# Performance work log

Hardware: AMD Instinct MI355X
Metric: run time of the kernel (lower is better)

The kernel has to match this reference:

```python
import jax, jax.numpy as jnp
import numpy as np

B, S, I, H = 64, 2048, 256, 256


def setup_inputs() -> dict:
    key = jax.random.key(0)
    ks = jax.random.split(key, 13)
    s_i = 1.0 / np.sqrt(I)
    s_h = 1.0 / np.sqrt(H)
    inp = {
        "input_seq": jax.random.normal(ks[0], (B, S, I), dtype=jnp.float32),
        "Wz": jax.random.uniform(ks[1], (I, H), jnp.float32, -s_i, s_i),
        "bz": jax.random.uniform(ks[2], (H,), jnp.float32, -s_i, s_i),
        "Wr": jax.random.uniform(ks[3], (I, H), jnp.float32, -s_i, s_i),
        "br": jax.random.uniform(ks[4], (H,), jnp.float32, -s_i, s_i),
        "Wh": jax.random.uniform(ks[5], (I, H), jnp.float32, -s_i, s_i),
        "bh": jax.random.uniform(ks[6], (H,), jnp.float32, -s_i, s_i),
        "Uz": jax.random.uniform(ks[7], (H, H), jnp.float32, -s_h, s_h),
        "buz": jax.random.uniform(ks[8], (H,), jnp.float32, -s_h, s_h),
        "Ur": jax.random.uniform(ks[9], (H, H), jnp.float32, -s_h, s_h),
        "bur": jax.random.uniform(ks[10], (H,), jnp.float32, -s_h, s_h),
        "Uh": jax.random.uniform(ks[11], (H, H), jnp.float32, -s_h, s_h),
        "buh": jax.random.uniform(ks[12], (H,), jnp.float32, -s_h, s_h),
    }
    return inp


def reference(input_seq, Wz, bz, Wr, br, Wh, bh, Uz, buz, Ur, bur, Uh, buh):
    # Precompute all input-side GEMMs in one batched pass: [B,S,H] each
    xz = jnp.einsum("bsi,ih->bsh", input_seq, Wz) + bz
    xr = jnp.einsum("bsi,ih->bsh", input_seq, Wr) + br
    xh = jnp.einsum("bsi,ih->bsh", input_seq, Wh) + bh
    # Time-major for scan: [S,B,H]
    xs = (xz.transpose(1, 0, 2), xr.transpose(1, 0, 2), xh.transpose(1, 0, 2))

    def step(h_prev, x_t):
        xz_t, xr_t, xh_t = x_t
        z = jax.nn.sigmoid(xz_t + h_prev @ Uz + buz)
        r = jax.nn.sigmoid(xr_t + h_prev @ Ur + bur)
        cand = jnp.tanh(xh_t + r * (h_prev @ Uh + buh))
        h_t = (1.0 - z) * h_prev + z * cand
        return h_t, h_t

    h0 = jnp.zeros((input_seq.shape[0], Uz.shape[0]), dtype=input_seq.dtype)
    _, hs = jax.lax.scan(step, h0, xs)  # hs: [S,B,H]
    return hs.transpose(1, 0, 2)  # [B,S,H]
```

## Files before the change

### kernel.cpp

```cpp
#include <hip/hip_runtime.h>
#include <hip/hip_bf16.h>
#include <hip/hip_fp16.h>


#define S_LEN 2048
#define BATCH 64
#define HDIM  256
#define NGATE 768
#define M_TOTAL (BATCH * S_LEN)

typedef _Float16 h8_t __attribute__((ext_vector_type(8)));
typedef float    f32x4 __attribute__((ext_vector_type(4)));
typedef int      i32x4 __attribute__((ext_vector_type(4)));

static __device__ __forceinline__ float h2f(unsigned short s) {
    _Float16 h; __builtin_memcpy(&h, &s, 2); return (float)h;
}
static __device__ __forceinline__ unsigned short f2h(float f) {
    _Float16 h = (_Float16)f; unsigned short s; __builtin_memcpy(&s, &h, 2); return s;
}

static __device__ __forceinline__ float sigmoid_fast(float x) {
    float e = __builtin_amdgcn_exp2f(-1.44269504088896341f * x);
    return __builtin_amdgcn_rcpf(1.0f + e);
}
static __device__ __forceinline__ float tanh_fast(float x) {
    return 2.0f * sigmoid_fast(2.0f * x) - 1.0f;
}


__global__ void k_cvt_x(const float4* __restrict__ x4, ushort4* __restrict__ xh4) {
    int i = blockIdx.x * blockDim.x + threadIdx.x;
    float4 v = x4[i];
    ushort4 o;
    o.x = f2h(v.x); o.y = f2h(v.y); o.z = f2h(v.z); o.w = f2h(v.w);
    xh4[i] = o;
}

__global__ void k_prep_w(const float* __restrict__ Wz, const float* __restrict__ Wr,
                         const float* __restrict__ Wh,
                         const float* __restrict__ bz, const float* __restrict__ br,
                         const float* __restrict__ bh,
                         const float* __restrict__ buz, const float* __restrict__ bur,
                         unsigned short* __restrict__ Wt, float* __restrict__ biascat) {
    int n = blockIdx.x;
    int k = threadIdx.x;
    int g = n >> 8, h = n & 255;
    const float* W = (g == 0) ? Wz : (g == 1) ? Wr : Wh;
    Wt[n * 256 + k] = f2h(W[k * 256 + h]);
    if (k == 0) {
        float bias = (g == 0) ? (bz[h] + buz[h]) : (g == 1) ? (br[h] + bur[h]) : bh[h];
        biascat[n] = bias;
    }
}

__global__ void k_prep_uq(const float* __restrict__ Uz, const float* __restrict__ Ur,
                          const float* __restrict__ Uh,
                          signed char* __restrict__ Ufrag, float* __restrict__ invU) {
    int blk = blockIdx.x;
    int g = blk >> 8, col = blk & 255;
    int k = threadIdx.x;
    const float* U = (g == 0) ? Uz : (g == 1) ? Ur : Uh;
    float v = U[k * 256 + col];
    __shared__ float red[256];
    red[k] = fabsf(v);
    __syncthreads();
    for (int off = 128; off > 0; off >>= 1) {
        if (k < off) red[k] = fmaxf(red[k], red[k + off]);
        __syncthreads();
    }
    float m = red[0];
    float s = (m > 0.0f) ? 127.0f / m : 0.0f;
    int q = __float2int_rn(v * s);
    q = max(-127, min(127, q));
    int ks = k >> 6, l4 = (k >> 4) & 3, e = k & 15;
    int l = l4 * 16 + (col & 15), nt = col >> 4;
    Ufrag[((size_t)(((g * 16 + nt) * 4 + ks) * 64 + l)) * 16 + e] = (signed char)q;
    if (k == 0) invU[g * 256 + col] = m * (1.0f / 16129.0f);
}


#define LDT 264

__global__ __launch_bounds__(256) void k_gemm_x(const unsigned short* __restrict__ Xh,
                                                const unsigned short* __restrict__ Wt,
                                                const float* __restrict__ biascat,
                                                unsigned short* __restrict__ XG) {
    __shared__ unsigned short As[128 * LDT];
    __shared__ unsigned short Bs[128 * LDT];
    int tid = threadIdx.x;
    int m0 = blockIdx.x * 128;
    int n0 = blockIdx.y * 128;

    {
        const unsigned short* ga = Xh + (size_t)m0 * 256;
        const unsigned short* gb = Wt + (size_t)n0 * 256;
#pragma unroll
        for (int i = 0; i < 16; i++) {
            int chunk = tid + i * 256;
            int row = chunk >> 5;
            int c8  = (chunk & 31) * 8;
            uint4 va = *(const uint4*)(ga + row * 256 + c8);
            *(uint4*)(As + row * LDT + c8) = va;
            uint4 vb = *(const uint4*)(gb + row * 256 + c8);
            *(uint4*)(Bs + row * LDT + c8) = vb;
        }
    }
    __syncthreads();

    int lane = tid & 63, wv = tid >> 6;
    int mw = (wv & 1) * 64, nw = (wv >> 1) * 64;
    int lr = lane & 15, lg = lane >> 4;

    f32x4 acc[4][4] = {};
#pragma unroll
    for (int k = 0; k < 8; k++) {
        h8_t a[4], b[4];
#pragma unroll
        for (int i = 0; i < 4; i++)
            a[i] = *(const h8_t*)(As + (mw + i * 16 + lr) * LDT + k * 32 + lg * 8);
#pragma unroll
        for (int jj = 0; jj < 4; jj++)
            b[jj] = *(const h8_t*)(Bs + (nw + jj * 16 + lr) * LDT + k * 32 + lg * 8);
#pragma unroll
        for (int i = 0; i < 4; i++)
#pragma unroll
            for (int jj = 0; jj < 4; jj++)
                acc[i][jj] = __builtin_amdgcn_mfma_f32_16x16x32_f16(a[i], b[jj], acc[i][jj], 0, 0, 0);
    }

#pragma unroll
    for (int jj = 0; jj < 4; jj++) {
        int gcol = n0 + nw + jj * 16 + lr;
        float bias = biascat[gcol];
#pragma unroll
        for (int i = 0; i < 4; i++) {
            int grow = m0 + mw + i * 16 + lg * 4;
#pragma unroll
            for (int r = 0; r < 4; r++) {
                XG[(size_t)(grow + r) * NGATE + gcol] = f2h(acc[i][jj][r] + bias);
            }
        }
    }
}


__global__ __launch_bounds__(512) __attribute__((amdgpu_waves_per_eu(2, 2)))
void k_gru(const i32x4* __restrict__ Ufrag,
           const float* __restrict__ invU,
           const unsigned short* __restrict__ XG,
           const float* __restrict__ buh,
           float* __restrict__ out) {
    __shared__ __align__(16) signed char hb[2][256];
    int tid = threadIdx.x;
    int lane = tid & 63, w = tid >> 6;
    int l4 = lane >> 4, lc = lane & 15;
    int b = blockIdx.x;
    int sel = l4 & 1;
    int c = (2 * w + sel) * 16 + lc;
    bool writer = (l4 < 2);

    i32x4 uf[3][2][4];
#pragma unroll
    for (int g = 0; g < 3; g++)
#pragma unroll
        for (int i = 0; i < 2; i++)
#pragma unroll
            for (int ks = 0; ks < 4; ks++)
                uf[g][i][ks] = Ufrag[(size_t)((g * 16 + (2 * w + i)) * 4 + ks) * 64 + lane];
#pragma unroll
    for (int g = 0; g < 3; g++)
#pragma unroll
        for (int i = 0; i < 2; i++)
#pragma unroll
            for (int ks = 0; ks < 4; ks++)
                asm volatile("" : "+v"(uf[g][i][ks]));

    i32x4 zc = {};
    asm volatile("" : "+v"(zc));

    float invz = invU[0 * 256 + c], invr = invU[1 * 256 + c], invh = invU[2 * 256 + c];
    float buh_c = buh[c];

    if (tid < 64) ((int*)hb[0])[tid] = 0;

    const unsigned short* xb = XG + (size_t)b * S_LEN * NGATE;
    float* ob = out + (size_t)b * S_LEN * HDIM;

    const unsigned short* xp = xb + c;
    unsigned short pz = xp[0], pr = xp[256], ph = xp[512];
    xp += NGATE;
    float hm = 0.0f;
    __syncthreads();

    for (int t = 0; t < S_LEN; ++t) {
        const signed char* hrow = hb[t & 1];
        signed char* hdst = hb[(t & 1) ^ 1];

        i32x4 acc[3][2];
        __builtin_amdgcn_s_setprio(1);
        {
            i32x4 a = *(const i32x4*)(hrow + l4 * 16);
#pragma unroll
            for (int g = 0; g < 3; g++)
#pragma unroll
                for (int i = 0; i < 2; i++)
                    acc[g][i] = __builtin_amdgcn_mfma_i32_16x16x64_i8(a, uf[g][i][0], zc, 0, 0, 0);
        }
#pragma unroll
        for (int ks = 1; ks < 4; ks++) {
            i32x4 a = *(const i32x4*)(hrow + ks * 64 + l4 * 16);
#pragma unroll
            for (int g = 0; g < 3; g++)
#pragma unroll
                for (int i = 0; i < 2; i++)
                    acc[g][i] = __builtin_amdgcn_mfma_i32_16x16x64_i8(a, uf[g][i][ks], acc[g][i], 0, 0, 0);
        }
        __builtin_amdgcn_s_setprio(0);

        float vz = (float)(sel ? acc[0][1][0] : acc[0][0][0]) * invz;
        float vr = (float)(sel ? acc[1][1][0] : acc[1][0][0]) * invr;
        float vh = (float)(sel ? acc[2][1][0] : acc[2][0][0]) * invh;

        float z = sigmoid_fast(h2f(pz) + vz);
        float r = sigmoid_fast(h2f(pr) + vr);
        float cd = tanh_fast(h2f(ph) + r * (vh + buh_c));
        hm = (1.0f - z) * hm + z * cd;

        if (writer) {
            ob[(size_t)t * HDIM + c] = hm;
            hdst[c] = (signed char)__float2int_rn(hm * 127.0f);
        }

        pz = xp[0]; pr = xp[256]; ph = xp[512];
        xp += NGATE;
        __syncthreads();
    }
}


extern "C" void kernel_launch(void* const* d_in, const int* in_sizes, int n_in,
                              void* d_out, int out_size, void* d_ws, size_t ws_size,
                              hipStream_t stream) {
    const float* x   = (const float*)d_in[0];
    const float* Wz  = (const float*)d_in[1];
    const float* bz  = (const float*)d_in[2];
    const float* Wr  = (const float*)d_in[3];
    const float* br  = (const float*)d_in[4];
    const float* Wh  = (const float*)d_in[5];
    const float* bh  = (const float*)d_in[6];
    const float* Uz  = (const float*)d_in[7];
    const float* buz = (const float*)d_in[8];
    const float* Ur  = (const float*)d_in[9];
    const float* bur = (const float*)d_in[10];
    const float* Uh  = (const float*)d_in[11];
    const float* buh = (const float*)d_in[12];

    char* ws = (char*)d_ws;
    unsigned short* Xh = (unsigned short*)(ws);
    unsigned short* XG = (unsigned short*)(ws + 67108864);
    unsigned short* Wt = (unsigned short*)(ws + 268435456);
    signed char*    Ufrag = (signed char*)(ws + 268828672);
    float*          biascat = (float*)(ws + 269221888);
    float*          invU = (float*)(ws + 269225984);

    k_cvt_x<<<32768, 256, 0, stream>>>((const float4*)x, (ushort4*)Xh);
    k_prep_w<<<768, 256, 0, stream>>>(Wz, Wr, Wh, bz, br, bh, buz, bur, Wt, biascat);
    k_prep_uq<<<768, 256, 0, stream>>>(Uz, Ur, Uh, Ufrag, invU);

    dim3 g1(M_TOTAL / 128, NGATE / 128);
    k_gemm_x<<<g1, 256, 0, stream>>>(Xh, Wt, biascat, XG);

    k_gru<<<BATCH, 512, 0, stream>>>((const i32x4*)Ufrag, invU, XG, buh, (float*)d_out);
}
```

Before: 1.282 ms.

## Fuse x fp16 conversion into input GEMM and prescale gate activations

Drops the separate fp32-to-fp16 conversion kernel: the input GEMM now reads x as fp32 and converts it while staging into LDS. Each block loops over all six N tiles and reuses the A tile instead of reloading it per N block. The -log2(e) and -2·log2(e) scale factors are folded into the precomputed gate inputs and the recurrent scales, which removes multiplies from the serial GRU step. The recurrent loop also prefetches gate inputs two steps ahead, loads all hidden-state fragments up front, and swaps __syncthreads for an explicit lgkmcnt wait plus s_barrier. Folding the scale before fp16 rounding slightly changes numerics, and the larger GEMM blocks have fewer blocks in flight.

```diff
diff --git a/kernel.cpp b/kernel.cpp
--- a/kernel.cpp
+++ b/kernel.cpp
@@ -20,22 +20,6 @@
     _Float16 h = (_Float16)f; unsigned short s; __builtin_memcpy(&s, &h, 2); return s;
 }
 
-static __device__ __forceinline__ float sigmoid_fast(float x) {
-    float e = __builtin_amdgcn_exp2f(-1.44269504088896341f * x);
-    return __builtin_amdgcn_rcpf(1.0f + e);
-}
-static __device__ __forceinline__ float tanh_fast(float x) {
-    return 2.0f * sigmoid_fast(2.0f * x) - 1.0f;
-}
-
-
-__global__ void k_cvt_x(const float4* __restrict__ x4, ushort4* __restrict__ xh4) {
-    int i = blockIdx.x * blockDim.x + threadIdx.x;
-    float4 v = x4[i];
-    ushort4 o;
-    o.x = f2h(v.x); o.y = f2h(v.y); o.z = f2h(v.z); o.w = f2h(v.w);
-    xh4[i] = o;
-}
 
 __global__ void k_prep_w(const float* __restrict__ Wz, const float* __restrict__ Wr,
                          const float* __restrict__ Wh,
@@ -82,7 +66,7 @@
 
 #define LDT 264
 
-__global__ __launch_bounds__(256) void k_gemm_x(const unsigned short* __restrict__ Xh,
+__global__ __launch_bounds__(256) void k_gemm_x(const float* __restrict__ x,
                                                 const unsigned short* __restrict__ Wt,
                                                 const float* __restrict__ biascat,
                                                 unsigned short* __restrict__ XG) {
@@ -90,55 +74,75 @@
     __shared__ unsigned short Bs[128 * LDT];
     int tid = threadIdx.x;
     int m0 = blockIdx.x * 128;
-    int n0 = blockIdx.y * 128;
 
     {
-        const unsigned short* ga = Xh + (size_t)m0 * 256;
-        const unsigned short* gb = Wt + (size_t)n0 * 256;
+        const float4* x4 = (const float4*)x;
 #pragma unroll
         for (int i = 0; i < 16; i++) {
             int chunk = tid + i * 256;
             int row = chunk >> 5;
             int c8  = (chunk & 31) * 8;
-            uint4 va = *(const uint4*)(ga + row * 256 + c8);
-            *(uint4*)(As + row * LDT + c8) = va;
-            uint4 vb = *(const uint4*)(gb + row * 256 + c8);
-            *(uint4*)(Bs + row * LDT + c8) = vb;
-        }
-    }
-    __syncthreads();
+            size_t fidx = (size_t)(m0 + row) * 64 + (c8 >> 2);
+            float4 va = x4[fidx];
+            float4 vb = x4[fidx + 1];
+            ushort4 o1, o2;
+            o1.x = f2h(va.x); o1.y = f2h(va.y); o1.z = f2h(va.z); o1.w = f2h(va.w);
+            o2.x = f2h(vb.x); o2.y = f2h(vb.y); o2.z = f2h(vb.z); o2.w = f2h(vb.w);
+            *(ushort4*)(As + row * LDT + c8) = o1;
+            *(ushort4*)(As + row * LDT + c8 + 4) = o2;
+        }
+    }
 
     int lane = tid & 63, wv = tid >> 6;
     int mw = (wv & 1) * 64, nw = (wv >> 1) * 64;
     int lr = lane & 15, lg = lane >> 4;
 
-    f32x4 acc[4][4] = {};
-#pragma unroll
-    for (int k = 0; k < 8; k++) {
-        h8_t a[4], b[4];
-#pragma unroll
-        for (int i = 0; i < 4; i++)
-            a[i] = *(const h8_t*)(As + (mw + i * 16 + lr) * LDT + k * 32 + lg * 8);
-#pragma unroll
-        for (int jj = 0; jj < 4; jj++)
-            b[jj] = *(const h8_t*)(Bs + (nw + jj * 16 + lr) * LDT + k * 32 + lg * 8);
-#pragma unroll
-        for (int i = 0; i < 4; i++)
+    for (int nb = 0; nb < 6; nb++) {
+        int n0 = nb * 128;
+        float gs = (nb < 4) ? -1.44269504f : -2.88539008f;
+
+        __syncthreads();
+        {
+            const unsigned short* gb = Wt + (size_t)n0 * 256;
+#pragma unroll
+            for (int i = 0; i < 16; i++) {
+                int chunk = tid + i * 256;
+                int row = chunk >> 5;
+                int c8  = (chunk & 31) * 8;
+                uint4 vb = *(const uint4*)(gb + row * 256 + c8);
+                *(uint4*)(Bs + row * LDT + c8) = vb;
+            }
+        }
+        __syncthreads();
+
+        f32x4 acc[4][4] = {};
+#pragma unroll
+        for (int k = 0; k < 8; k++) {
+            h8_t a[4], b[4];
+#pragma unroll
+            for (int i = 0; i < 4; i++)
+                a[i] = *(const h8_t*)(As + (mw + i * 16 + lr) * LDT + k * 32 + lg * 8);
 #pragma unroll
             for (int jj = 0; jj < 4; jj++)
-                acc[i][jj] = __builtin_amdgcn_mfma_f32_16x16x32_f16(a[i], b[jj], acc[i][jj], 0, 0, 0);
-    }
-
-#pragma unroll
-    for (int jj = 0; jj < 4; jj++) {
-        int gcol = n0 + nw + jj * 16 + lr;
-        float bias = biascat[gcol];
-#pragma unroll
-        for (int i = 0; i < 4; i++) {
-            int grow = m0 + mw + i * 16 + lg * 4;
-#pragma unroll
-            for (int r = 0; r < 4; r++) {
-                XG[(size_t)(grow + r) * NGATE + gcol] = f2h(acc[i][jj][r] + bias);
+                b[jj] = *(const h8_t*)(Bs + (nw + jj * 16 + lr) * LDT + k * 32 + lg * 8);
+#pragma unroll
+            for (int i = 0; i < 4; i++)
+#pragma unroll
+                for (int jj = 0; jj < 4; jj++)
+                    acc[i][jj] = __builtin_amdgcn_mfma_f32_16x16x32_f16(a[i], b[jj], acc[i][jj], 0, 0, 0);
+        }
+
+#pragma unroll
+        for (int jj = 0; jj < 4; jj++) {
+            int gcol = n0 + nw + jj * 16 + lr;
+            float bias = biascat[gcol];
+#pragma unroll
+            for (int i = 0; i < 4; i++) {
+                int grow = m0 + mw + i * 16 + lg * 4;
+#pragma unroll
+                for (int r = 0; r < 4; r++) {
+                    XG[(size_t)(grow + r) * NGATE + gcol] = f2h((acc[i][jj][r] + bias) * gs);
+                }
             }
         }
     }
@@ -179,17 +183,19 @@
     i32x4 zc = {};
     asm volatile("" : "+v"(zc));
 
-    float invz = invU[0 * 256 + c], invr = invU[1 * 256 + c], invh = invU[2 * 256 + c];
-    float buh_c = buh[c];
+    float invz = -1.44269504f * invU[0 * 256 + c];
+    float invr = -1.44269504f * invU[1 * 256 + c];
+    float invh = -2.88539008f * invU[2 * 256 + c];
+    float buh_c = -2.88539008f * buh[c];
 
     if (tid < 64) ((int*)hb[0])[tid] = 0;
 
     const unsigned short* xb = XG + (size_t)b * S_LEN * NGATE;
     float* ob = out + (size_t)b * S_LEN * HDIM;
 
-    const unsigned short* xp = xb + c;
-    unsigned short pz = xp[0], pr = xp[256], ph = xp[512];
-    xp += NGATE;
+    const unsigned short* xq = xb + c;
+    unsigned short xcz = xq[0], xcr = xq[256], xch = xq[512]; xq += NGATE;
+    unsigned short xnz = xq[0], xnr = xq[256], xnh = xq[512]; xq += NGATE;
     float hm = 0.0f;
     __syncthreads();
 
@@ -197,44 +203,59 @@
         const signed char* hrow = hb[t & 1];
         signed char* hdst = hb[(t & 1) ^ 1];
 
+        const i32x4* hq = (const i32x4*)hrow;
+        i32x4 a0 = hq[l4];
+        i32x4 a1 = hq[4 + l4];
+        i32x4 a2 = hq[8 + l4];
+        i32x4 a3 = hq[12 + l4];
+
         i32x4 acc[3][2];
         __builtin_amdgcn_s_setprio(1);
-        {
-            i32x4 a = *(const i32x4*)(hrow + l4 * 16);
-#pragma unroll
-            for (int g = 0; g < 3; g++)
-#pragma unroll
-                for (int i = 0; i < 2; i++)
-                    acc[g][i] = __builtin_amdgcn_mfma_i32_16x16x64_i8(a, uf[g][i][0], zc, 0, 0, 0);
-        }
-#pragma unroll
-        for (int ks = 1; ks < 4; ks++) {
-            i32x4 a = *(const i32x4*)(hrow + ks * 64 + l4 * 16);
-#pragma unroll
-            for (int g = 0; g < 3; g++)
-#pragma unroll
-                for (int i = 0; i < 2; i++)
-                    acc[g][i] = __builtin_amdgcn_mfma_i32_16x16x64_i8(a, uf[g][i][ks], acc[g][i], 0, 0, 0);
-        }
+#pragma unroll
+        for (int g = 0; g < 3; g++)
+#pragma unroll
+            for (int i = 0; i < 2; i++)
+                acc[g][i] = __builtin_amdgcn_mfma_i32_16x16x64_i8(a0, uf[g][i][0], zc, 0, 0, 0);
+#pragma unroll
+        for (int g = 0; g < 3; g++)
+#pragma unroll
+            for (int i = 0; i < 2; i++)
+                acc[g][i] = __builtin_amdgcn_mfma_i32_16x16x64_i8(a1, uf[g][i][1], acc[g][i], 0, 0, 0);
+#pragma unroll
+        for (int g = 0; g < 3; g++)
+#pragma unroll
+            for (int i = 0; i < 2; i++)
+                acc[g][i] = __builtin_amdgcn_mfma_i32_16x16x64_i8(a2, uf[g][i][2], acc[g][i], 0, 0, 0);
+#pragma unroll
+        for (int g = 0; g < 3; g++)
+#pragma unroll
+            for (int i = 0; i < 2; i++)
+                acc[g][i] = __builtin_amdgcn_mfma_i32_16x16x64_i8(a3, uf[g][i][3], acc[g][i], 0, 0, 0);
         __builtin_amdgcn_s_setprio(0);
 
         float vz = (float)(sel ? acc[0][1][0] : acc[0][0][0]) * invz;
         float vr = (float)(sel ? acc[1][1][0] : acc[1][0][0]) * invr;
         float vh = (float)(sel ? acc[2][1][0] : acc[2][0][0]) * invh;
 
-        float z = sigmoid_fast(h2f(pz) + vz);
-        float r = sigmoid_fast(h2f(pr) + vr);
-        float cd = tanh_fast(h2f(ph) + r * (vh + buh_c));
-        hm = (1.0f - z) * hm + z * cd;
+        float ez = __builtin_amdgcn_exp2f(h2f(xcz) + vz);
+        float z  = __builtin_amdgcn_rcpf(1.0f + ez);
+        float er = __builtin_amdgcn_exp2f(h2f(xcr) + vr);
+        float r  = __builtin_amdgcn_rcpf(1.0f + er);
+        float eh = __builtin_amdgcn_exp2f(h2f(xch) + r * (vh + buh_c));
+        float cd = 2.0f * __builtin_amdgcn_rcpf(1.0f + eh) - 1.0f;
+        hm = hm + z * (cd - hm);
 
         if (writer) {
             ob[(size_t)t * HDIM + c] = hm;
             hdst[c] = (signed char)__float2int_rn(hm * 127.0f);
         }
 
-        pz = xp[0]; pr = xp[256]; ph = xp[512];
-        xp += NGATE;
-        __syncthreads();
+        xcz = xnz; xcr = xnr; xch = xnh;
+        xnz = xq[0]; xnr = xq[256]; xnh = xq[512];
+        xq += NGATE;
+
+        asm volatile("s_waitcnt lgkmcnt(0)" ::: "memory");
+        __builtin_amdgcn_s_barrier();
     }
 }
 
@@ -257,19 +278,16 @@
     const float* buh = (const float*)d_in[12];
 
     char* ws = (char*)d_ws;
-    unsigned short* Xh = (unsigned short*)(ws);
     unsigned short* XG = (unsigned short*)(ws + 67108864);
     unsigned short* Wt = (unsigned short*)(ws + 268435456);
     signed char*    Ufrag = (signed char*)(ws + 268828672);
     float*          biascat = (float*)(ws + 269221888);
     float*          invU = (float*)(ws + 269225984);
 
-    k_cvt_x<<<32768, 256, 0, stream>>>((const float4*)x, (ushort4*)Xh);
     k_prep_w<<<768, 256, 0, stream>>>(Wz, Wr, Wh, bz, br, bh, buz, bur, Wt, biascat);
     k_prep_uq<<<768, 256, 0, stream>>>(Uz, Ur, Uh, Ufrag, invU);
 
-    dim3 g1(M_TOTAL / 128, NGATE / 128);
-    k_gemm_x<<<g1, 256, 0, stream>>>(Xh, Wt, biascat, XG);
+    k_gemm_x<<<M_TOTAL / 128, 256, 0, stream>>>(x, Wt, biascat, XG);
 
     k_gru<<<BATCH, 512, 0, stream>>>((const i32x4*)Ufrag, invU, XG, buh, (float*)d_out);
 }
```

Result: slower. 1.913 ms (+49.2%).
